# Performance work log

Measured on AMD Instinct MI355X. Metric: run time of the kernel, lower is better.

## Reference

```python
import jax, jax.numpy as jnp
import numpy as np

B, S, D = 1, 2048, 4096
NH, NKV, HD = 32, 8, 128          # n_heads, n_kv_heads, head_dim
N_REP = NH // NKV                  # repeat_kv factor (GQA)
ROPE_THETA = 10000.0


def setup_inputs() -> dict:
    key = jax.random.key(0)
    ks = jax.random.split(key, 5)
    x = jax.random.normal(ks[0], (B, S, D), jnp.float32)
    wq = jax.random.normal(ks[1], (D, NH * HD), jnp.float32) * (1.0 / np.sqrt(D))
    wk = jax.random.normal(ks[2], (D, NKV * HD), jnp.float32) * (1.0 / np.sqrt(D))
    wv = jax.random.normal(ks[3], (D, NKV * HD), jnp.float32) * (1.0 / np.sqrt(D))
    wo = jax.random.normal(ks[4], (NH * HD, D), jnp.float32) * (1.0 / np.sqrt(NH * HD))
    # freqs_cis = exp(i * t * theta^{-2j/hd}); store as cos/sin, shape (S, HD//2)
    inv_freq = 1.0 / (ROPE_THETA ** (np.arange(0, HD, 2, dtype=np.float32) / HD))
    angles = np.outer(np.arange(S, dtype=np.float32), inv_freq)
    return {"x": x, "wq": wq, "wk": wk, "wv": wv, "wo": wo,
            "cos": jnp.asarray(np.cos(angles), jnp.float32),
            "sin": jnp.asarray(np.sin(angles), jnp.float32)}


def _rope(t, cos, sin):
    # t: (b, s, h, hd); pairs (t[...,2j], t[...,2j+1]) form complex numbers
    tr, ti = t[..., 0::2], t[..., 1::2]
    c = cos[None, :, None, :]
    s = sin[None, :, None, :]
    out = jnp.stack([tr * c - ti * s, tr * s + ti * c], axis=-1)  # re-interleave
    return out.reshape(t.shape)


def reference(x, wq, wk, wv, wo, cos, sin):
    b, s, _ = x.shape
    q = (x @ wq).reshape(b, s, NH, HD)
    k = (x @ wk).reshape(b, s, NKV, HD)
    v = (x @ wv).reshape(b, s, NKV, HD)
    q = _rope(q, cos, sin)
    k = _rope(k, cos, sin)
    # prefill with start_pos=0: KV cache slice == fresh k, v
    # repeat_kv == torch.repeat_interleave along head dim
    k = jnp.repeat(k, N_REP, axis=2)  # (b, s, NH, HD)
    v = jnp.repeat(v, N_REP, axis=2)
    q = q.transpose(0, 2, 1, 3)  # (b, NH, s, hd)
    k = k.transpose(0, 2, 1, 3)
    v = v.transpose(0, 2, 1, 3)
    scores = jnp.einsum('bhqd,bhkd->bhqk', q, k) / jnp.sqrt(jnp.float32(HD))
    causal = jnp.tril(jnp.ones((s, s), bool))
    scores = jnp.where(causal[None, None], scores, jnp.float32(-1e30))
    probs = jax.nn.softmax(scores, axis=-1)
    out = jnp.einsum('bhqk,bhkd->bhqd', probs, v)
    out = out.transpose(0, 2, 1, 3).reshape(b, s, NH * HD)
    return out @ wo
```

## Files before the change

### kernel.cpp

```cpp
#include <hip/hip_runtime.h>
#include <stdint.h>

typedef unsigned short ushort_t;
typedef short bf16x4 __attribute__((ext_vector_type(4)));
typedef short bf16x8 __attribute__((ext_vector_type(8)));
typedef float f32x4 __attribute__((ext_vector_type(4)));
typedef float f32x16 __attribute__((ext_vector_type(16)));
typedef float f32x4v __attribute__((ext_vector_type(4)));

__device__ __forceinline__ ushort_t f2bf(float f) {
  unsigned int u = __builtin_bit_cast(unsigned int, f);
  u += 0x7fffu + ((u >> 16) & 1u);
  return (ushort_t)(u >> 16);
}
__device__ __forceinline__ float bf2f(ushort_t h) {
  unsigned int u = ((unsigned int)h) << 16;
  return __builtin_bit_cast(float, u);
}
__device__ __forceinline__ float exp2_hw(float x) {
  return __builtin_amdgcn_exp2f(x);
}
__device__ __forceinline__ void load_lds16(const void* g, void* l) {
  __builtin_amdgcn_global_load_lds(
      (const __attribute__((address_space(1))) void*)g,
      (__attribute__((address_space(3))) void*)l, 16, 0, 0);
}

__global__ __launch_bounds__(256) void cvt_x_kernel(const float* __restrict__ x,
                                                    ushort_t* __restrict__ xb) {
  int i = blockIdx.x * 256 + threadIdx.x;
  const f32x4v* xv = (const f32x4v*)x;
  f32x4v a = xv[2 * i], b = xv[2 * i + 1];
  bf16x8 o;
  o[0] = (short)f2bf(a[0]); o[1] = (short)f2bf(a[1]);
  o[2] = (short)f2bf(a[2]); o[3] = (short)f2bf(a[3]);
  o[4] = (short)f2bf(b[0]); o[5] = (short)f2bf(b[1]);
  o[6] = (short)f2bf(b[2]); o[7] = (short)f2bf(b[3]);
  ((bf16x8*)xb)[i] = o;
}

__global__ __launch_bounds__(256) void tr_cvt_kernel(const float* __restrict__ src,
                                                     ushort_t* __restrict__ dst,
                                                     int R, int C) {
  __shared__ float tile[64][65];
  int r0 = blockIdx.y * 64, c0 = blockIdx.x * 64;
  int t = threadIdx.x;
#pragma unroll
  for (int i = 0; i < 16; i++) {
    int idx = t + i * 256;
    int r = idx >> 6, c = idx & 63;
    tile[r][c] = src[(size_t)(r0 + r) * C + c0 + c];
  }
  __syncthreads();
#pragma unroll
  for (int i = 0; i < 16; i++) {
    int idx = t + i * 256;
    int cr = idx >> 6, cc = idx & 63;
    dst[(size_t)(c0 + cr) * R + r0 + cc] = f2bf(tile[cc][cr]);
  }
}

__global__ __launch_bounds__(256) void rope_kernel(ushort_t* __restrict__ C1,
                                                   const float* __restrict__ cosb,
                                                   const float* __restrict__ sinb) {
  int idx = blockIdx.x * 256 + threadIdx.x;
  int s = idx / 640;
  int col0 = (idx % 640) * 8;
  int i0 = (col0 & 127) >> 1;
  const float qs = (col0 < 4096) ? 0.12753055296570565f : 1.0f;
  ushort_t* p = C1 + (size_t)s * 6144 + col0;
  bf16x8 v = *(const bf16x8*)p;
  bf16x8 o;
  const float* cr = cosb + s * 64 + i0;
  const float* sr = sinb + s * 64 + i0;
#pragma unroll
  for (int j = 0; j < 4; j++) {
    float tr = bf2f((ushort_t)v[2 * j]);
    float ti = bf2f((ushort_t)v[2 * j + 1]);
    float c = cr[j], sn = sr[j];
    o[2 * j] = (short)f2bf((tr * c - ti * sn) * qs);
    o[2 * j + 1] = (short)f2bf((tr * sn + ti * c) * qs);
  }
  *(bf16x8*)p = o;
}

__global__ __launch_bounds__(256) void trv_kernel(const ushort_t* __restrict__ C1,
                                                  ushort_t* __restrict__ VT) {
  __shared__ ushort_t tile[64][65];
  int c0 = blockIdx.x * 64;
  int r0 = blockIdx.y * 64;
  int t = threadIdx.x;
#pragma unroll
  for (int i = 0; i < 16; i++) {
    int idx = t + i * 256;
    int r = idx >> 6, c = idx & 63;
    tile[r][c] = C1[(size_t)(r0 + r) * 6144 + 5120 + c0 + c];
  }
  __syncthreads();
#pragma unroll
  for (int i = 0; i < 16; i++) {
    int idx = t + i * 256;
    int cr = idx >> 6, cc = idx & 63;
    VT[(size_t)(c0 + cr) * 2048 + r0 + cc] = tile[cc][cr];
  }
}

__device__ __forceinline__ void xcd_chunk_map(int id, int nby, int nbx,
                                              int& browi, int& bcoli) {
  const int xcd = id & 7;
  const int j = id >> 3;
  const int rch = nby >> 1, cch = nbx >> 2;
  const int cr = xcd >> 2, cc = xcd & 3;
  const int r = j / cch, c = j % cch;
  browi = cr * rch + r;
  bcoli = cc * cch + c;
}

template <typename OutT>
__global__ __launch_bounds__(512) void gemmC_kernel(const ushort_t* __restrict__ A,
                                                    const ushort_t* __restrict__ BT,
                                                    OutT* __restrict__ C,
                                                    int M, int N, int K, int ldc) {
  __shared__ ushort_t As[2][256 * 64];
  __shared__ ushort_t Bs[2][192 * 64];
  const int nbx = N / 192, nby = M >> 8;
  int browi, bcoli;
  xcd_chunk_map((int)blockIdx.x, nby, nbx, browi, bcoli);
  const int brow = browi << 8, bcol = bcoli * 192;
  const int tid = threadIdx.x, w = tid >> 6, lane = tid & 63;
  const int wr = w >> 2, wc = w & 3;
  const int lr = lane & 15, lk = lane >> 4;

  const ushort_t* Ab = A + (size_t)brow * K;
  const ushort_t* Bb = BT + (size_t)bcol * K;

  auto stageQ = [&](const ushort_t* gbase, char* lds, int t, int q) {
    int L = q * 512 + tid;
    int r = L >> 3, sc = L & 7;
    load_lds16(gbase + (size_t)r * K + (t << 6) + ((sc ^ (r & 7)) << 3), lds + L * 16);
  };

  f32x4 acc[8][3] = {};
  const int NT = K >> 6;

#pragma unroll
  for (int q = 0; q < 4; ++q) stageQ(Ab, (char*)&As[0][0], 0, q);
#pragma unroll
  for (int q = 0; q < 3; ++q) stageQ(Bb, (char*)&Bs[0][0], 0, q);
  asm volatile("s_waitcnt vmcnt(0)" ::: "memory");
  __builtin_amdgcn_s_barrier();

  for (int t = 0; t < NT; ++t) {
    const int c = t & 1;
    const char* Ac = (const char*)&As[c][0];
    const char* Bc = (const char*)&Bs[c][0];
    char* An = (char*)&As[c ^ 1][0];
    char* Bn = (char*)&Bs[c ^ 1][0];
    const bool pf = (t + 1 < NT);

    bf16x8 af[4][2], bfr[3][2];
#pragma unroll
    for (int mm = 0; mm < 4; ++mm)
#pragma unroll
      for (int ks = 0; ks < 2; ++ks) {
        int rA = wr * 128 + mm * 16 + lr;
        af[mm][ks] = *(const bf16x8*)(Ac + rA * 128 + (((ks * 4 + lk) ^ (rA & 7)) << 4));
      }
#pragma unroll
    for (int n = 0; n < 2; ++n)
#pragma unroll
      for (int ks = 0; ks < 2; ++ks) {
        int rB = wc * 48 + n * 16 + lr;
        bfr[n][ks] = *(const bf16x8*)(Bc + rB * 128 + (((ks * 4 + lk) ^ (rB & 7)) << 4));
      }
    if (pf) { stageQ(Ab, An, t + 1, 0); stageQ(Ab, An, t + 1, 2); }
    __builtin_amdgcn_s_barrier();
    asm volatile("s_waitcnt lgkmcnt(0)" ::: "memory");
    __builtin_amdgcn_sched_barrier(0);
    __builtin_amdgcn_s_setprio(1);
#pragma unroll
    for (int mm = 0; mm < 4; ++mm)
#pragma unroll
      for (int n = 0; n < 2; ++n)
#pragma unroll
        for (int ks = 0; ks < 2; ++ks)
          acc[mm][n] = __builtin_amdgcn_mfma_f32_16x16x32_bf16(af[mm][ks], bfr[n][ks],
                                                               acc[mm][n], 0, 0, 0);
    __builtin_amdgcn_s_setprio(0);
    __builtin_amdgcn_s_barrier();

#pragma unroll
    for (int ks = 0; ks < 2; ++ks) {
      int rB = wc * 48 + 32 + lr;
      bfr[2][ks] = *(const bf16x8*)(Bc + rB * 128 + (((ks * 4 + lk) ^ (rB & 7)) << 4));
    }
    if (pf) { stageQ(Bb, Bn, t + 1, 0); stageQ(Bb, Bn, t + 1, 1); }
    __builtin_amdgcn_s_barrier();
    asm volatile("s_waitcnt lgkmcnt(0)" ::: "memory");
    __builtin_amdgcn_sched_barrier(0);
    __builtin_amdgcn_s_setprio(1);
#pragma unroll
    for (int mm = 0; mm < 4; ++mm)
#pragma unroll
      for (int ks = 0; ks < 2; ++ks)
        acc[mm][2] = __builtin_amdgcn_mfma_f32_16x16x32_bf16(af[mm][ks], bfr[2][ks],
                                                             acc[mm][2], 0, 0, 0);
    __builtin_amdgcn_s_setprio(0);
    asm volatile("s_waitcnt vmcnt(4)" ::: "memory");
    __builtin_amdgcn_s_barrier();

#pragma unroll
    for (int mm = 0; mm < 4; ++mm)
#pragma unroll
      for (int ks = 0; ks < 2; ++ks) {
        int rA = wr * 128 + 64 + mm * 16 + lr;
        af[mm][ks] = *(const bf16x8*)(Ac + rA * 128 + (((ks * 4 + lk) ^ (rA & 7)) << 4));
      }
    if (pf) { stageQ(Bb, Bn, t + 1, 2); stageQ(Ab, An, t + 1, 1); }
    __builtin_amdgcn_s_barrier();
    asm volatile("s_waitcnt lgkmcnt(0)" ::: "memory");
    __builtin_amdgcn_sched_barrier(0);
    __builtin_amdgcn_s_setprio(1);
#pragma unroll
    for (int mm = 0; mm < 4; ++mm)
#pragma unroll
      for (int n = 0; n < 2; ++n)
#pragma unroll
        for (int ks = 0; ks < 2; ++ks)
          acc[4 + mm][n] = __builtin_amdgcn_mfma_f32_16x16x32_bf16(af[mm][ks], bfr[n][ks],
                                                                   acc[4 + mm][n], 0, 0, 0);
    __builtin_amdgcn_s_setprio(0);
    __builtin_amdgcn_s_barrier();

    if (pf) stageQ(Ab, An, t + 1, 3);
    __builtin_amdgcn_s_setprio(1);
#pragma unroll
    for (int mm = 0; mm < 4; ++mm)
#pragma unroll
      for (int ks = 0; ks < 2; ++ks)
        acc[4 + mm][2] = __builtin_amdgcn_mfma_f32_16x16x32_bf16(af[mm][ks], bfr[2][ks],
                                                                 acc[4 + mm][2], 0, 0, 0);
    __builtin_amdgcn_s_setprio(0);
    asm volatile("s_waitcnt vmcnt(2)" ::: "memory");
    __builtin_amdgcn_s_barrier();
  }
#pragma unroll
  for (int m = 0; m < 8; ++m)
#pragma unroll
    for (int n = 0; n < 3; ++n) {
      int row = brow + wr * 128 + m * 16 + lk * 4;
      int col = bcol + wc * 48 + n * 16 + lr;
#pragma unroll
      for (int j = 0; j < 4; ++j) {
        float v = acc[m][n][j];
        if constexpr (sizeof(OutT) == 2)
          C[(size_t)(row + j) * ldc + col] = (OutT)f2bf(v);
        else
          C[(size_t)(row + j) * ldc + col] = v;
      }
    }
}

template <typename OutT>
__global__ __launch_bounds__(512) void gemmB_kernel(const ushort_t* __restrict__ A,
                                                    const ushort_t* __restrict__ BT,
                                                    OutT* __restrict__ C,
                                                    int M, int N, int K, int ldc) {
  __shared__ ushort_t As[3][128 * 64];
  __shared__ ushort_t Bs[3][256 * 64];
  const int nbx = N >> 8, nby = M >> 7;
  int browi, bcoli;
  xcd_chunk_map((int)blockIdx.x, nby, nbx, browi, bcoli);
  const int brow = browi << 7, bcol = bcoli << 8;
  const int tid = threadIdx.x, w = tid >> 6, lane = tid & 63;
  const int wr = w >> 2, wc = w & 3;
  const int lr = lane & 15, lk = lane >> 4;

  const ushort_t* Ab = A + (size_t)brow * K;
  const ushort_t* Bb = BT + (size_t)bcol * K;

  auto stageQ = [&](const ushort_t* gbase, char* lds, int t, int q) {
    int L = q * 512 + tid;
    int r = L >> 3, sc = L & 7;
    load_lds16(gbase + (size_t)r * K + (t << 6) + ((sc ^ (r & 7)) << 3), lds + L * 16);
  };
  auto stageTile = [&](int t, int buf) {
    stageQ(Ab, (char*)&As[buf][0], t, 0);
    stageQ(Ab, (char*)&As[buf][0], t, 1);
#pragma unroll
    for (int q = 0; q < 4; ++q) stageQ(Bb, (char*)&Bs[buf][0], t, q);
  };

  f32x4 acc[4][4] = {};
  const int NT = K >> 6;

  stageTile(0, 0);
  stageTile(1, 1);
  asm volatile("s_waitcnt vmcnt(6)" ::: "memory");
  __builtin_amdgcn_s_barrier();

  int cur = 0;
  for (int t = 0; t < NT; ++t) {
    const char* Ac = (const char*)&As[cur][0];
    const char* Bc = (const char*)&Bs[cur][0];
    const int nxt = (cur + 2 >= 3) ? cur - 1 : cur + 2;
    char* An = (char*)&As[nxt][0];
    char* Bn = (char*)&Bs[nxt][0];
    const bool pf = (t + 2 < NT);

    bf16x8 af[4][2], bfr[4][2];
#pragma unroll
    for (int mm = 0; mm < 2; ++mm)
#pragma unroll
      for (int ks = 0; ks < 2; ++ks) {
        int rA = wr * 64 + mm * 16 + lr;
        af[mm][ks] = *(const bf16x8*)(Ac + rA * 128 + (((ks * 4 + lk) ^ (rA & 7)) << 4));
      }
#pragma unroll
    for (int n = 0; n < 2; ++n)
#pragma unroll
      for (int ks = 0; ks < 2; ++ks) {
        int rB = wc * 64 + n * 16 + lr;
        bfr[n][ks] = *(const bf16x8*)(Bc + rB * 128 + (((ks * 4 + lk) ^ (rB & 7)) << 4));
      }
    if (pf) stageQ(Ab, An, t + 2, 0);
    __builtin_amdgcn_s_barrier();
    asm volatile("s_waitcnt lgkmcnt(0)" ::: "memory");
    __builtin_amdgcn_sched_barrier(0);
    __builtin_amdgcn_s_setprio(1);
#pragma unroll
    for (int mm = 0; mm < 2; ++mm)
#pragma unroll
      for (int n = 0; n < 2; ++n)
#pragma unroll
        for (int ks = 0; ks < 2; ++ks)
          acc[mm][n] = __builtin_amdgcn_mfma_f32_16x16x32_bf16(af[mm][ks], bfr[n][ks],
                                                               acc[mm][n], 0, 0, 0);
    __builtin_amdgcn_s_setprio(0);
    __builtin_amdgcn_s_barrier();

#pragma unroll
    for (int n = 2; n < 4; ++n)
#pragma unroll
      for (int ks = 0; ks < 2; ++ks) {
        int rB = wc * 64 + n * 16 + lr;
        bfr[n][ks] = *(const bf16x8*)(Bc + rB * 128 + (((ks * 4 + lk) ^ (rB & 7)) << 4));
      }
    if (pf) stageQ(Ab, An, t + 2, 1);
    __builtin_amdgcn_s_barrier();
    asm volatile("s_waitcnt lgkmcnt(0)" ::: "memory");
    __builtin_amdgcn_sched_barrier(0);
    __builtin_amdgcn_s_setprio(1);
#pragma unroll
    for (int mm = 0; mm < 2; ++mm)
#pragma unroll
      for (int n = 2; n < 4; ++n)
#pragma unroll
        for (int ks = 0; ks < 2; ++ks)
          acc[mm][n] = __builtin_amdgcn_mfma_f32_16x16x32_bf16(af[mm][ks], bfr[n][ks],
                                                               acc[mm][n], 0, 0, 0);
    __builtin_amdgcn_s_setprio(0);
    __builtin_amdgcn_s_barrier();

#pragma unroll
    for (int mm = 0; mm < 2; ++mm)
#pragma unroll
      for (int ks = 0; ks < 2; ++ks) {
        int rA = wr * 64 + (mm + 2) * 16 + lr;
        af[2 + mm][ks] = *(const bf16x8*)(Ac + rA * 128 + (((ks * 4 + lk) ^ (rA & 7)) << 4));
      }
    if (pf) { stageQ(Bb, Bn, t + 2, 0); stageQ(Bb, Bn, t + 2, 1); }
    __builtin_amdgcn_s_barrier();
    asm volatile("s_waitcnt lgkmcnt(0)" ::: "memory");
    __builtin_amdgcn_sched_barrier(0);
    __builtin_amdgcn_s_setprio(1);
#pragma unroll
    for (int mm = 0; mm < 2; ++mm)
#pragma unroll
      for (int n = 0; n < 2; ++n)
#pragma unroll
        for (int ks = 0; ks < 2; ++ks)
          acc[2 + mm][n] = __builtin_amdgcn_mfma_f32_16x16x32_bf16(af[2 + mm][ks], bfr[n][ks],
                                                                   acc[2 + mm][n], 0, 0, 0);
    __builtin_amdgcn_s_setprio(0);
    __builtin_amdgcn_s_barrier();

    if (pf) { stageQ(Bb, Bn, t + 2, 2); stageQ(Bb, Bn, t + 2, 3); }
    __builtin_amdgcn_s_setprio(1);
#pragma unroll
    for (int mm = 0; mm < 2; ++mm)
#pragma unroll
      for (int n = 2; n < 4; ++n)
#pragma unroll
        for (int ks = 0; ks < 2; ++ks)
          acc[2 + mm][n] = __builtin_amdgcn_mfma_f32_16x16x32_bf16(af[2 + mm][ks], bfr[n][ks],
                                                                   acc[2 + mm][n], 0, 0, 0);
    __builtin_amdgcn_s_setprio(0);
    if (pf)
      asm volatile("s_waitcnt vmcnt(6)" ::: "memory");
    else if (t + 1 < NT)
      asm volatile("s_waitcnt vmcnt(0)" ::: "memory");
    __builtin_amdgcn_s_barrier();
    cur = (cur == 2) ? 0 : cur + 1;
  }
#pragma unroll
  for (int m = 0; m < 4; ++m)
#pragma unroll
    for (int n = 0; n < 4; ++n) {
      int row = brow + wr * 64 + m * 16 + lk * 4;
      int col = bcol + wc * 64 + n * 16 + lr;
#pragma unroll
      for (int j = 0; j < 4; ++j) {
        float v = acc[m][n][j];
        if constexpr (sizeof(OutT) == 2)
          C[(size_t)(row + j) * ldc + col] = (OutT)f2bf(v);
        else
          C[(size_t)(row + j) * ldc + col] = v;
      }
    }
}

template <typename OutT>
__global__ __launch_bounds__(256) void gemm128_kernel(const ushort_t* __restrict__ A,
                                                      const ushort_t* __restrict__ BT,
                                                      OutT* __restrict__ C,
                                                      int M, int N, int K, int ldc) {
  __shared__ ushort_t As[128 * 32];
  __shared__ ushort_t Bs[128 * 32];
  int brow = blockIdx.y * 128, bcol = blockIdx.x * 128;
  int tid = threadIdx.x, w = tid >> 6, lane = tid & 63;
  int wr = w >> 1, wc = w & 1;
  int lr = lane & 15, lk = lane >> 4;
  f32x4 acc[4][4] = {};

  int srow = lane >> 2;
  int scol = (lane & 3) * 8;
  const ushort_t* Ab = A + (size_t)brow * K + scol;
  const ushort_t* Bb = BT + (size_t)bcol * K + scol;

  for (int kt = 0; kt < K; kt += 32) {
#pragma unroll
    for (int i = 0; i < 2; i++) {
      int seg = w * 2 + i;
      int row = seg * 16 + srow;
      load_lds16(Ab + (size_t)row * K + kt, (char*)As + seg * 1024);
      load_lds16(Bb + (size_t)row * K + kt, (char*)Bs + seg * 1024);
    }
    __syncthreads();
    bf16x8 af[4], bfr[4];
#pragma unroll
    for (int m = 0; m < 4; m++)
      af[m] = *(const bf16x8*)&As[(wr * 64 + m * 16 + lr) * 32 + lk * 8];
#pragma unroll
    for (int n = 0; n < 4; n++)
      bfr[n] = *(const bf16x8*)&Bs[(wc * 64 + n * 16 + lr) * 32 + lk * 8];
#pragma unroll
    for (int m = 0; m < 4; m++)
#pragma unroll
      for (int n = 0; n < 4; n++)
        acc[m][n] = __builtin_amdgcn_mfma_f32_16x16x32_bf16(af[m], bfr[n], acc[m][n], 0, 0, 0);
    __syncthreads();
  }
#pragma unroll
  for (int m = 0; m < 4; m++)
#pragma unroll
    for (int n = 0; n < 4; n++) {
      int row = brow + wr * 64 + m * 16 + lk * 4;
      int col = bcol + wc * 64 + n * 16 + lr;
#pragma unroll
      for (int j = 0; j < 4; j++) {
        float v = acc[m][n][j];
        if constexpr (sizeof(OutT) == 2)
          C[(size_t)(row + j) * ldc + col] = (OutT)f2bf(v);
        else
          C[(size_t)(row + j) * ldc + col] = v;
      }
    }
}

__global__ __launch_bounds__(256) void gemmS_kernel(const ushort_t* __restrict__ C1,
                                                    ushort_t* __restrict__ P) {
  int rem = blockIdx.x, rt = 0;
  while (rem > rt) { rem -= (rt + 1); rt++; }
  const int ct = rem;
  const int h = blockIdx.y, hk = h >> 2;

  __shared__ ushort_t As[128 * 32];
  __shared__ ushort_t Bs[128 * 32];
  int tid = threadIdx.x, w = tid >> 6, lane = tid & 63;
  int wr = w >> 1, wc = w & 1;
  int lr = lane & 15, lk = lane >> 4;
  f32x4 acc[4][4] = {};
  int srow = lane >> 2;
  int scol = (lane & 3) * 8;
  const ushort_t* Ab = C1 + (size_t)(rt * 128) * 6144 + h * 128 + scol;
  const ushort_t* Bb = C1 + (size_t)(ct * 128) * 6144 + 4096 + hk * 128 + scol;

  for (int kt = 0; kt < 128; kt += 32) {
#pragma unroll
    for (int i = 0; i < 2; i++) {
      int seg = w * 2 + i;
      int row = seg * 16 + srow;
      load_lds16(Ab + (size_t)row * 6144 + kt, (char*)As + seg * 1024);
      load_lds16(Bb + (size_t)row * 6144 + kt, (char*)Bs + seg * 1024);
    }
    __syncthreads();
    bf16x8 af[4], bfr[4];
#pragma unroll
    for (int m = 0; m < 4; m++)
      af[m] = *(const bf16x8*)&As[(wr * 64 + m * 16 + lr) * 32 + lk * 8];
#pragma unroll
    for (int n = 0; n < 4; n++)
      bfr[n] = *(const bf16x8*)&Bs[(wc * 64 + n * 16 + lr) * 32 + lk * 8];
#pragma unroll
    for (int m = 0; m < 4; m++)
#pragma unroll
      for (int n = 0; n < 4; n++)
        acc[m][n] = __builtin_amdgcn_mfma_f32_16x16x32_bf16(af[m], bfr[n], acc[m][n], 0, 0, 0);
    __syncthreads();
  }
  ushort_t* Pt = P + ((size_t)h * 136 + (size_t)(rt * (rt + 1) / 2) + ct) * 16384;
  const bool diag = (rt == ct);
#pragma unroll
  for (int m = 0; m < 4; m++)
#pragma unroll
    for (int n = 0; n < 4; n++) {
      int row = wr * 64 + m * 16 + lk * 4;
      int col = wc * 64 + n * 16 + lr;
#pragma unroll
      for (int j = 0; j < 4; j++) {
        float v = exp2_hw(acc[m][n][j]);
        if (diag && col > row + j) v = 0.f;
        Pt[(row + j) * 128 + col] = f2bf(v);
      }
    }
}

__global__ __launch_bounds__(256) void gemmPV_kernel(const ushort_t* __restrict__ P,
                                                     const ushort_t* __restrict__ VT,
                                                     ushort_t* __restrict__ AO) {
  const int h = blockIdx.x, hk = h >> 2;
  const int rt = 15 - (int)blockIdx.y;

  __shared__ ushort_t As[128 * 32];
  __shared__ ushort_t Bs[128 * 32];
  int tid = threadIdx.x, w = tid >> 6, lane = tid & 63;
  int wr = w >> 1, wc = w & 1;
  int lr = lane & 15, lk = lane >> 4;
  f32x4 acc[4][4] = {};
  f32x4 sacc[4] = {};
  bf16x8 ones;
#pragma unroll
  for (int j = 0; j < 8; j++) ones[j] = (short)0x3F80;
  int srow = lane >> 2;
  int scol = (lane & 3) * 8;
  const ushort_t* Ph = P + ((size_t)h * 136 + (size_t)(rt * (rt + 1) / 2)) * 16384;
  const ushort_t* Vh = VT + (size_t)hk * 128 * 2048;

  const int nks = (rt + 1) * 4;
  for (int ks = 0; ks < nks; ks++) {
    int k0 = ks * 32;
    int ctk = k0 >> 7, kin = k0 & 127;
#pragma unroll
    for (int i = 0; i < 2; i++) {
      int seg = w * 2 + i;
      int row = seg * 16 + srow;
      load_lds16(Ph + (size_t)ctk * 16384 + (size_t)row * 128 + kin + scol,
                 (char*)As + seg * 1024);
      load_lds16(Vh + (size_t)row * 2048 + k0 + scol, (char*)Bs + seg * 1024);
    }
    __syncthreads();
    bf16x8 af[4], bfr[4];
#pragma unroll
    for (int m = 0; m < 4; m++)
      af[m] = *(const bf16x8*)&As[(wr * 64 + m * 16 + lr) * 32 + lk * 8];
#pragma unroll
    for (int n = 0; n < 4; n++)
      bfr[n] = *(const bf16x8*)&Bs[(wc * 64 + n * 16 + lr) * 32 + lk * 8];
#pragma unroll
    for (int m = 0; m < 4; m++) {
#pragma unroll
      for (int n = 0; n < 4; n++)
        acc[m][n] = __builtin_amdgcn_mfma_f32_16x16x32_bf16(af[m], bfr[n], acc[m][n], 0, 0, 0);
      sacc[m] = __builtin_amdgcn_mfma_f32_16x16x32_bf16(af[m], ones, sacc[m], 0, 0, 0);
    }
    __syncthreads();
  }
  const int q0 = rt * 128;
#pragma unroll
  for (int m = 0; m < 4; m++) {
    float invs[4];
#pragma unroll
    for (int j = 0; j < 4; j++) invs[j] = 1.0f / sacc[m][j];
#pragma unroll
    for (int n = 0; n < 4; n++) {
      int row = wr * 64 + m * 16 + lk * 4;
      int col = wc * 64 + n * 16 + lr;
#pragma unroll
      for (int j = 0; j < 4; j++) {
        float v = acc[m][n][j] * invs[j];
        AO[(size_t)(q0 + row + j) * 4096 + h * 128 + col] = f2bf(v);
      }
    }
  }
}

__global__ __launch_bounds__(256) void fattn_kernel(const ushort_t* __restrict__ C1,
                                                    const ushort_t* __restrict__ VT,
                                                    ushort_t* __restrict__ AO) {
  __shared__ ushort_t Pl[4][32][72];
  const int h = blockIdx.x, hk = h >> 2;
  const int qt = gridDim.y - 1 - blockIdx.y;
  const int tid = threadIdx.x, w = tid >> 6, lane = tid & 63;
  const int lq = lane & 31, hi = lane >> 5;
  const int qw0 = qt * 128 + w * 32;
  const int qabs = qw0 + lq;

  const ushort_t* Kb = C1 + 4096 + (size_t)hk * 128;
  const ushort_t* Vb = VT + (size_t)hk * 128 * 2048;

  bf16x8 qf[8];
  {
    const ushort_t* qrow = C1 + (size_t)qabs * 6144 + h * 128;
#pragma unroll
    for (int s = 0; s < 8; s++) qf[s] = *(const bf16x8*)(qrow + s * 16 + hi * 8);
  }
  f32x16 ot[4] = {};
  float mrow = -1e30f, ssum = 0.f;

  const int ktmax = (qw0 + 31) >> 6;
  for (int kt = 0; kt <= ktmax; kt++) {
    f32x16 sg[2] = {};
#pragma unroll
    for (int g = 0; g < 2; g++) {
      bf16x8 kfa[8];
      const ushort_t* krow = Kb + (size_t)(kt * 64 + g * 32 + lq) * 6144 + hi * 8;
#pragma unroll
      for (int s = 0; s < 8; s++) kfa[s] = *(const bf16x8*)(krow + s * 16);
#pragma unroll
      for (int s = 0; s < 8; s++)
        sg[g] = __builtin_amdgcn_mfma_f32_32x32x16_bf16(kfa[s], qf[s], sg[g], 0, 0, 0);
    }
    if (kt * 64 + 63 > qw0) {
#pragma unroll
      for (int g = 0; g < 2; g++)
#pragma unroll
        for (int r = 0; r < 16; r++) {
          int key = kt * 64 + g * 32 + (r & 3) + 8 * (r >> 2) + 4 * hi;
          if (key > qabs) sg[g][r] = -1e30f;
        }
    }
    float pm = -1e30f;
#pragma unroll
    for (int g = 0; g < 2; g++)
#pragma unroll
      for (int r = 0; r < 16; r++) pm = fmaxf(pm, sg[g][r]);
    pm = fmaxf(pm, __shfl_xor(pm, 32));
    float mnew = fmaxf(mrow, pm);
    float corr = exp2_hw(mrow - mnew);
    mrow = mnew;
    float ps = 0.f;
#pragma unroll
    for (int g = 0; g < 2; g++)
#pragma unroll
      for (int r = 0; r < 16; r++) {
        float e = exp2_hw(sg[g][r] - mnew);
        sg[g][r] = e;
        ps += e;
      }
    ps += __shfl_xor(ps, 32);
    ssum = ssum * corr + ps;
    if (!__all(corr == 1.f)) {
#pragma unroll
      for (int d = 0; d < 4; d++)
#pragma unroll
        for (int r = 0; r < 16; r++) ot[d][r] *= corr;
    }
#pragma unroll
    for (int g = 0; g < 2; g++)
#pragma unroll
      for (int rq = 0; rq < 4; rq++) {
        bf16x4 pk;
#pragma unroll
        for (int j = 0; j < 4; j++) pk[j] = (short)f2bf(sg[g][rq * 4 + j]);
        *(bf16x4*)&Pl[w][lq][g * 32 + rq * 8 + hi * 4] = pk;
      }
    asm volatile("s_waitcnt lgkmcnt(0)" ::: "memory");
    bf16x8 pf[4];
#pragma unroll
    for (int s = 0; s < 4; s++) pf[s] = *(const bf16x8*)&Pl[w][lq][s * 16 + hi * 8];
#pragma unroll
    for (int d = 0; d < 4; d++) {
      bf16x8 vfa[4];
      const ushort_t* vrow = Vb + (size_t)(d * 32 + lq) * 2048 + kt * 64 + hi * 8;
#pragma unroll
      for (int s = 0; s < 4; s++) vfa[s] = *(const bf16x8*)(vrow + s * 16);
#pragma unroll
      for (int s = 0; s < 4; s++)
        ot[d] = __builtin_amdgcn_mfma_f32_32x32x16_bf16(vfa[s], pf[s], ot[d], 0, 0, 0);
    }
  }
  const float inv = 1.0f / ssum;
  ushort_t* orow = AO + (size_t)qabs * 4096 + h * 128;
#pragma unroll
  for (int d = 0; d < 4; d++)
#pragma unroll
    for (int rq = 0; rq < 4; rq++) {
      bf16x4 ok;
#pragma unroll
      for (int j = 0; j < 4; j++) ok[j] = (short)f2bf(ot[d][rq * 4 + j] * inv);
      *(bf16x4*)(orow + d * 32 + rq * 8 + hi * 4) = ok;
    }
}

extern "C" void kernel_launch(void* const* d_in, const int* in_sizes, int n_in,
                              void* d_out, int out_size, void* d_ws, size_t ws_size,
                              hipStream_t stream) {
  (void)in_sizes; (void)n_in; (void)out_size;
  const float* x    = (const float*)d_in[0];
  const float* wq   = (const float*)d_in[1];
  const float* wk   = (const float*)d_in[2];
  const float* wv   = (const float*)d_in[3];
  const float* wo   = (const float*)d_in[4];
  const float* cosb = (const float*)d_in[5];
  const float* sinb = (const float*)d_in[6];

  char* ws = (char*)d_ws;
  const bool fast = ws_size >= (215ull << 20);

  if (fast) {
    ushort_t* C1  = (ushort_t*)(ws);
    ushort_t* VT  = (ushort_t*)(ws + ((size_t)24 << 20));
    ushort_t* woT = (ushort_t*)(ws + ((size_t)28 << 20));
    ushort_t* xb  = (ushort_t*)(ws + ((size_t)60 << 20));
    ushort_t* wT  = (ushort_t*)(ws + ((size_t)76 << 20));
    ushort_t* P   = (ushort_t*)(ws + ((size_t)60 << 20));
    ushort_t* AO  = (ushort_t*)(ws + ((size_t)196 << 20));

    cvt_x_kernel<<<4096, 256, 0, stream>>>(x, xb);
    tr_cvt_kernel<<<dim3(64, 64), 256, 0, stream>>>(wq, wT, 4096, 4096);
    tr_cvt_kernel<<<dim3(16, 64), 256, 0, stream>>>(wk, wT + (size_t)4096 * 4096, 4096, 1024);
    tr_cvt_kernel<<<dim3(16, 64), 256, 0, stream>>>(wv, wT + (size_t)5120 * 4096, 4096, 1024);
    tr_cvt_kernel<<<dim3(64, 64), 256, 0, stream>>>(wo, woT, 4096, 4096);

    gemmC_kernel<ushort_t><<<256, 512, 0, stream>>>(xb, wT, C1, 2048, 6144, 4096, 6144);
    rope_kernel<<<5120, 256, 0, stream>>>(C1, cosb, sinb);
    trv_kernel<<<dim3(16, 32), 256, 0, stream>>>(C1, VT);

    gemmS_kernel<<<dim3(136, 32), 256, 0, stream>>>(C1, P);
    gemmPV_kernel<<<dim3(32, 16), 256, 0, stream>>>(P, VT, AO);

    gemmB_kernel<float><<<256, 512, 0, stream>>>(AO, woT, (float*)d_out, 2048, 4096, 4096, 4096);
  } else {
    ushort_t* xb  = (ushort_t*)(ws);
    ushort_t* wT  = (ushort_t*)(ws + ((size_t)16 << 20));
    ushort_t* C1  = (ushort_t*)(ws + ((size_t)64 << 20));
    ushort_t* VT  = (ushort_t*)(ws + ((size_t)88 << 20));
    ushort_t* AO  = xb;
    ushort_t* woT = wT;

    cvt_x_kernel<<<4096, 256, 0, stream>>>(x, xb);
    tr_cvt_kernel<<<dim3(64, 64), 256, 0, stream>>>(wq, wT, 4096, 4096);
    tr_cvt_kernel<<<dim3(16, 64), 256, 0, stream>>>(wk, wT + (size_t)4096 * 4096, 4096, 1024);
    tr_cvt_kernel<<<dim3(16, 64), 256, 0, stream>>>(wv, wT + (size_t)5120 * 4096, 4096, 1024);
    gemm128_kernel<ushort_t><<<dim3(48, 16), 256, 0, stream>>>(xb, wT, C1, 2048, 6144, 4096, 6144);
    rope_kernel<<<5120, 256, 0, stream>>>(C1, cosb, sinb);
    trv_kernel<<<dim3(16, 32), 256, 0, stream>>>(C1, VT);
    tr_cvt_kernel<<<dim3(64, 64), 256, 0, stream>>>(wo, woT, 4096, 4096);
    fattn_kernel<<<dim3(32, 16), 256, 0, stream>>>(C1, VT, AO);
    gemm128_kernel<float><<<dim3(32, 16), 256, 0, stream>>>(AO, woT, (float*)d_out, 2048, 4096, 4096, 4096);
  }
}
```

Baseline: 377.7 us.

## Triple-buffer B tiles in GEMM to prefetch two K-steps ahead; vectorize transpose-convert

The GEMM now keeps three LDS buffers for the B operand and prefetches B two K-iterations ahead while A stays double-buffered one step ahead, with the vmcnt waits retuned to match. This is meant to hide more global-load latency behind the MFMA work. It raises LDS use per block, which may lower occupancy. Separately, the transpose-convert kernel switches to float4 loads and bf16x4 stores to cut memory instructions.

```diff
diff --git a/kernel.cpp b/kernel.cpp
--- a/kernel.cpp
+++ b/kernel.cpp
@@ -46,17 +46,22 @@
   int r0 = blockIdx.y * 64, c0 = blockIdx.x * 64;
   int t = threadIdx.x;
 #pragma unroll
-  for (int i = 0; i < 16; i++) {
+  for (int i = 0; i < 4; i++) {
     int idx = t + i * 256;
-    int r = idx >> 6, c = idx & 63;
-    tile[r][c] = src[(size_t)(r0 + r) * C + c0 + c];
+    int r = idx >> 4, c4 = idx & 15;
+    f32x4v v = *(const f32x4v*)&src[(size_t)(r0 + r) * C + c0 + c4 * 4];
+#pragma unroll
+    for (int j = 0; j < 4; j++) tile[r][c4 * 4 + j] = v[j];
   }
   __syncthreads();
 #pragma unroll
-  for (int i = 0; i < 16; i++) {
+  for (int i = 0; i < 4; i++) {
     int idx = t + i * 256;
-    int cr = idx >> 6, cc = idx & 63;
-    dst[(size_t)(c0 + cr) * R + r0 + cc] = f2bf(tile[cc][cr]);
+    int cr = idx >> 4, cg = idx & 15;
+    bf16x4 o;
+#pragma unroll
+    for (int j = 0; j < 4; j++) o[j] = (short)f2bf(tile[cg * 4 + j][cr]);
+    *(bf16x4*)&dst[(size_t)(c0 + cr) * R + r0 + cg * 4] = o;
   }
 }
 
@@ -122,7 +127,7 @@
                                                     OutT* __restrict__ C,
                                                     int M, int N, int K, int ldc) {
   __shared__ ushort_t As[2][256 * 64];
-  __shared__ ushort_t Bs[2][192 * 64];
+  __shared__ ushort_t Bs[3][192 * 64];
   const int nbx = N / 192, nby = M >> 8;
   int browi, bcoli;
   xcd_chunk_map((int)blockIdx.x, nby, nbx, browi, bcoli);
@@ -144,19 +149,25 @@
   const int NT = K >> 6;
 
 #pragma unroll
-  for (int q = 0; q < 4; ++q) stageQ(Ab, (char*)&As[0][0], 0, q);
-#pragma unroll
   for (int q = 0; q < 3; ++q) stageQ(Bb, (char*)&Bs[0][0], 0, q);
-  asm volatile("s_waitcnt vmcnt(0)" ::: "memory");
+  stageQ(Ab, (char*)&As[0][0], 0, 0);
+  stageQ(Ab, (char*)&As[0][0], 0, 2);
+  stageQ(Ab, (char*)&As[0][0], 0, 1);
+  stageQ(Ab, (char*)&As[0][0], 0, 3);
+#pragma unroll
+  for (int q = 0; q < 3; ++q) stageQ(Bb, (char*)&Bs[1][0], 1, q);
+  asm volatile("s_waitcnt vmcnt(5)" ::: "memory");
   __builtin_amdgcn_s_barrier();
 
+  int bcur = 0;
   for (int t = 0; t < NT; ++t) {
     const int c = t & 1;
     const char* Ac = (const char*)&As[c][0];
-    const char* Bc = (const char*)&Bs[c][0];
+    const char* Bc = (const char*)&Bs[bcur][0];
     char* An = (char*)&As[c ^ 1][0];
-    char* Bn = (char*)&Bs[c ^ 1][0];
-    const bool pf = (t + 1 < NT);
+    const int bnxt = (bcur + 2 >= 3) ? bcur - 1 : bcur + 2;
+    char* Bn = (char*)&Bs[bnxt][0];
+    const bool pfA = (t + 1 < NT), pfB = (t + 2 < NT);
 
     bf16x8 af[4][2], bfr[3][2];
 #pragma unroll
@@ -173,7 +184,7 @@
         int rB = wc * 48 + n * 16 + lr;
         bfr[n][ks] = *(const bf16x8*)(Bc + rB * 128 + (((ks * 4 + lk) ^ (rB & 7)) << 4));
       }
-    if (pf) { stageQ(Ab, An, t + 1, 0); stageQ(Ab, An, t + 1, 2); }
+    if (pfA) { stageQ(Ab, An, t + 1, 0); stageQ(Ab, An, t + 1, 2); }
     __builtin_amdgcn_s_barrier();
     asm volatile("s_waitcnt lgkmcnt(0)" ::: "memory");
     __builtin_amdgcn_sched_barrier(0);
@@ -194,7 +205,7 @@
       int rB = wc * 48 + 32 + lr;
       bfr[2][ks] = *(const bf16x8*)(Bc + rB * 128 + (((ks * 4 + lk) ^ (rB & 7)) << 4));
     }
-    if (pf) { stageQ(Bb, Bn, t + 1, 0); stageQ(Bb, Bn, t + 1, 1); }
+    if (pfA) { stageQ(Ab, An, t + 1, 1); stageQ(Ab, An, t + 1, 3); }
     __builtin_amdgcn_s_barrier();
     asm volatile("s_waitcnt lgkmcnt(0)" ::: "memory");
     __builtin_amdgcn_sched_barrier(0);
@@ -206,7 +217,7 @@
         acc[mm][2] = __builtin_amdgcn_mfma_f32_16x16x32_bf16(af[mm][ks], bfr[2][ks],
                                                              acc[mm][2], 0, 0, 0);
     __builtin_amdgcn_s_setprio(0);
-    asm volatile("s_waitcnt vmcnt(4)" ::: "memory");
+    asm volatile("s_waitcnt vmcnt(7)" ::: "memory");
     __builtin_amdgcn_s_barrier();
 
 #pragma unroll
@@ -216,7 +227,7 @@
         int rA = wr * 128 + 64 + mm * 16 + lr;
         af[mm][ks] = *(const bf16x8*)(Ac + rA * 128 + (((ks * 4 + lk) ^ (rA & 7)) << 4));
       }
-    if (pf) { stageQ(Bb, Bn, t + 1, 2); stageQ(Ab, An, t + 1, 1); }
+    if (pfB) { stageQ(Bb, Bn, t + 2, 0); stageQ(Bb, Bn, t + 2, 1); }
     __builtin_amdgcn_s_barrier();
     asm volatile("s_waitcnt lgkmcnt(0)" ::: "memory");
     __builtin_amdgcn_sched_barrier(0);
@@ -232,7 +243,7 @@
     __builtin_amdgcn_s_setprio(0);
     __builtin_amdgcn_s_barrier();
 
-    if (pf) stageQ(Ab, An, t + 1, 3);
+    if (pfB) stageQ(Bb, Bn, t + 2, 2);
     __builtin_amdgcn_s_setprio(1);
 #pragma unroll
     for (int mm = 0; mm < 4; ++mm)
@@ -241,8 +252,12 @@
         acc[4 + mm][2] = __builtin_amdgcn_mfma_f32_16x16x32_bf16(af[mm][ks], bfr[2][ks],
                                                                  acc[4 + mm][2], 0, 0, 0);
     __builtin_amdgcn_s_setprio(0);
-    asm volatile("s_waitcnt vmcnt(2)" ::: "memory");
-    __builtin_amdgcn_s_barrier();
+    if (pfB)
+      asm volatile("s_waitcnt vmcnt(5)" ::: "memory");
+    else
+      asm volatile("s_waitcnt vmcnt(0)" ::: "memory");
+    __builtin_amdgcn_s_barrier();
+    bcur = (bcur + 1 == 3) ? 0 : bcur + 1;
   }
 #pragma unroll
   for (int m = 0; m < 8; ++m)
```

Result: no change. 373.4 us (-1.2%).
